# Optimization experiments

Measured on AMD Instinct MI355X. Metric: run time of the kernel, lower is better.

## Reference

```python
import jax, jax.numpy as jnp
import numpy as np

DT = 0.01      # timestep
RE = 0.001     # 'Re' coefficient in source
NLEVEL = 5     # multigrid levels
D, H, W = 96, 192, 192  # nz, ny, nx interior grid


def _conv(x, w, stride=1):
    # 1->1 channel 3D stencil conv, VALID padding (matches Conv3d padding=0, bias=0)
    return jax.lax.conv_general_dilated(
        x, w, (stride,) * 3, 'VALID',
        dimension_numbers=('NCDHW', 'OIDHW', 'NCDHW'))


def _pad(x):
    # BC application + halo exchange collapsed to zero halo (single-device reference)
    return jnp.pad(x, ((0, 0), (0, 0), (1, 1), (1, 1), (1, 1)))


def _prol(x):
    # nn.Upsample(scale_factor=2, mode='nearest')
    for ax in (2, 3, 4):
        x = jnp.repeat(x, 2, axis=ax)
    return x


def _stencils():
    wA = np.zeros((1, 1, 3, 3, 3), np.float32)
    wA[0, 0, 1, 1, 1] = -6.0
    for d in range(3):
        idx = [1, 1, 1]
        idx[d] = 0; wA[(0, 0, *idx)] = 1.0
        idx[d] = 2; wA[(0, 0, *idx)] = 1.0
    w_diff = wA.copy()
    w_x = np.zeros((1, 1, 3, 3, 3), np.float32); w_x[0, 0, 1, 1, 0] = -0.5; w_x[0, 0, 1, 1, 2] = 0.5
    w_y = np.zeros((1, 1, 3, 3, 3), np.float32); w_y[0, 0, 1, 0, 1] = -0.5; w_y[0, 0, 1, 2, 1] = 0.5
    w_z = np.zeros((1, 1, 3, 3, 3), np.float32); w_z[0, 0, 0, 1, 1] = -0.5; w_z[0, 0, 2, 1, 1] = 0.5
    w_res = np.full((1, 1, 2, 2, 2), 0.125, np.float32)
    return tuple(jnp.asarray(a) for a in (wA, w_diff, w_x, w_y, w_z, w_res))


def setup_inputs() -> dict:
    key = jax.random.key(0)
    ks = jax.random.split(key, 5)
    shape = (1, 1, D, H, W)
    wA, w_diff, w_xadv, w_yadv, w_zadv, w_res = _stencils()
    return {
        'values_u': jax.random.normal(ks[0], shape, jnp.float32),
        'values_v': jax.random.normal(ks[1], shape, jnp.float32),
        'values_w': jax.random.normal(ks[2], shape, jnp.float32),
        'values_p': jax.random.normal(ks[3], shape, jnp.float32),
        'sigma': jax.random.uniform(ks[4], shape, jnp.float32),
        'wA': wA, 'w_diff': w_diff, 'w_xadv': w_xadv,
        'w_yadv': w_yadv, 'w_zadv': w_zadv, 'w_res': w_res,
        'iteration': 2,
    }


def _forward(values_u, values_v, values_w, values_p, sigma,
             wA, w_diff, w_xadv, w_yadv, w_zadv, w_res, iteration):
    diag = wA[0, 0, 1, 1, 1]
    A = lambda x: _conv(x, wA)
    diff = lambda x: _conv(x, w_diff)
    xadv = lambda x: _conv(x, w_xadv)
    yadv = lambda x: _conv(x, w_yadv)
    zadv = lambda x: _conv(x, w_zadv)
    res = lambda x: _conv(x, w_res, stride=2)

    inv = 1.0 / (1.0 + DT * sigma)           # solid_body (LIBM) damping
    sb = lambda a, b, c: (a * inv, b * inv, c * inv)

    def pg(uu, vv, ww, u, v, w_):
        # PG_vector with k_u = k_v = k_w = ones
        kpp = _pad(jnp.ones_like(u))
        ku = 0.5 * (diff(uu) + diff(uu * kpp) - u * diff(kpp))
        kv = 0.5 * (diff(vv) + diff(vv * kpp) - v * diff(kpp))
        kw = 0.5 * (diff(ww) + diff(ww * kpp) - w_ * diff(kpp))
        return ku, kv, kw

    u, v, w_ = sb(values_u, values_v, values_w)
    uu, vv, ww, pp = _pad(u), _pad(v), _pad(w_), _pad(values_p)

    ku, kv, kw = pg(uu, vv, ww, u, v, w_)
    b_u = u + 0.5 * (RE * ku * DT - u * xadv(uu) * DT - v * yadv(uu) * DT - w_ * zadv(uu) * DT) - xadv(pp) * DT
    b_v = v + 0.5 * (RE * kv * DT - u * xadv(vv) * DT - v * yadv(vv) * DT - w_ * zadv(vv) * DT) - yadv(pp) * DT
    b_w = w_ + 0.5 * (RE * kw * DT - u * xadv(ww) * DT - v * yadv(ww) * DT - w_ * zadv(ww) * DT) - zadv(pp) * DT
    b_u, b_v, b_w = sb(b_u, b_v, b_w)
    buu, bvv, bww = _pad(b_u), _pad(b_v), _pad(b_w)

    ku, kv, kw = pg(buu, bvv, bww, b_u, b_v, b_w)
    u = u + RE * ku * DT - b_u * xadv(buu) * DT - b_v * yadv(buu) * DT - b_w * zadv(buu) * DT - xadv(pp) * DT
    v = v + RE * kv * DT - b_u * xadv(bvv) * DT - b_v * yadv(bvv) * DT - b_w * zadv(bvv) * DT - yadv(pp) * DT
    w_ = w_ + RE * kw * DT - b_u * xadv(bww) * DT - b_v * yadv(bww) * DT - b_w * zadv(bww) * DT - zadv(pp) * DT
    u, v, w_ = sb(u, v, w_)
    uu, vv, ww = _pad(u), _pad(v), _pad(w_)

    # F_cycle_MG: multigrid pressure solve
    b = -(xadv(uu) + yadv(vv) + zadv(ww)) / DT
    p = values_p
    for _ in range(iteration):
        wmg = jnp.zeros((1, 1, 1, 1, 1), p.dtype)
        r = A(pp) - b
        r_s = [r]
        for _i in range(1, NLEVEL - 1):
            r = res(r)
            r_s.append(r)
        for i in reversed(range(1, NLEVEL - 1)):
            wmg = wmg - A(_pad(wmg)) / diag + r_s[i] / diag  # Jacobi smooth (broadcasts at coarsest)
            wmg = _prol(wmg)
        p = p - wmg
        p = p - A(pp) / diag + b / diag
        pp = _pad(p)

    u = u - xadv(pp) * DT
    v = v - yadv(pp) * DT
    w_ = w_ - zadv(pp) * DT
    u, v, w_ = sb(u, v, w_)
    return u, v, w_, p, wmg, r


def reference(values_u, values_v, values_w, values_p, sigma,
              wA, w_diff, w_xadv, w_yadv, w_zadv, w_res, iteration):
    return _forward(values_u, values_v, values_w, values_p, sigma,
                    wA, w_diff, w_xadv, w_yadv, w_zadv, w_res, iteration)
```

## Files before the change

kernel.cpp:

```cpp
#include <hip/hip_runtime.h>

#define DZc 96
#define HYc 192
#define WXc 192
#define SHs (WXc)
#define SDs (HYc*WXc)
#define NTOT (DZc*HYc*WXc)
#define DTc 0.01f
#define REc 0.001f

#define D1 48
#define H1 96
#define W1 96
#define N1 (D1*H1*W1)
#define D2 24
#define H2 48
#define W2 48
#define N2 (D2*H2*W2)
#define D3 12
#define H3 24
#define W3 24
#define N3 (D3*H3*W3)


struct Row6 { float a[6]; };

struct Geo {
  int base, il, ir, iym, iyp, izm, izp;
  float mxl, mxr, mym, myp, mzm, mzp;
};

__device__ __forceinline__ Geo mkgeo(int x0,int y,int z){
  Geo g;
  g.base = (z*HYc + y)*WXc + x0;
  bool hxm=x0>0, hxp=x0<WXc-4, hym=y>0, hyp=y<HYc-1, hzm=z>0, hzp=z<DZc-1;
  g.il  = hxm ? g.base-1   : g.base;  g.ir  = hxp ? g.base+4   : g.base;
  g.iym = hym ? g.base-SHs : g.base;  g.iyp = hyp ? g.base+SHs : g.base;
  g.izm = hzm ? g.base-SDs : g.base;  g.izp = hzp ? g.base+SDs : g.base;
  g.mxl = hxm?1.f:0.f; g.mxr = hxp?1.f:0.f;
  g.mym = hym?1.f:0.f; g.myp = hyp?1.f:0.f;
  g.mzm = hzm?1.f:0.f; g.mzp = hzp?1.f:0.f;
  return g;
}

__device__ __forceinline__ Row6 ld6(const float* __restrict__ f, const Geo& g){
  Row6 r;
  float4 c = *reinterpret_cast<const float4*>(f + g.base);
  r.a[0]=f[g.il]*g.mxl; r.a[1]=c.x; r.a[2]=c.y; r.a[3]=c.z; r.a[4]=c.w; r.a[5]=f[g.ir]*g.mxr;
  return r;
}
__device__ __forceinline__ void ld4a(const float* __restrict__ f, int idx, float* o){
  float4 c = *reinterpret_cast<const float4*>(f + idx);
  o[0]=c.x; o[1]=c.y; o[2]=c.z; o[3]=c.w;
}

struct Sten { Row6 c; float ym[4], yp[4], zm[4], zp[4]; };
__device__ __forceinline__ Sten ldsten(const float* __restrict__ f, const Geo& g){
  Sten s;
  s.c = ld6(f,g);
  ld4a(f,g.iym,s.ym); ld4a(f,g.iyp,s.yp); ld4a(f,g.izm,s.zm); ld4a(f,g.izp,s.zp);
  return s;
}

__device__ __forceinline__ void restrict_body(
    const float rv[4], int x0,
    float (*l0)[4][192], float (*l1)[2][96],
    float* __restrict__ r1p, float* __restrict__ r2p,
    int by, int bz){
  *reinterpret_cast<float4*>(&l0[threadIdx.z][threadIdx.y][x0]) =
      make_float4(rv[0],rv[1],rv[2],rv[3]);
  __syncthreads();
  int t = (threadIdx.z*4 + threadIdx.y)*48 + threadIdx.x;
  if (t < 384){
    int xc = t % 96, yc = (t/96)&1, zc = t/192;
    float s = 0.f;
    for (int a=0;a<2;a++)
      for (int bq=0;bq<2;bq++)
        s += l0[2*zc+a][2*yc+bq][2*xc] + l0[2*zc+a][2*yc+bq][2*xc+1];
    float r1v = 0.125f*s;
    r1p[((bz*2+zc)*H1 + (by*2+yc))*W1 + xc] = r1v;
    l1[zc][yc][xc] = r1v;
  }
  __syncthreads();
  if (t < 48){
    float s = 0.f;
    for (int a=0;a<2;a++)
      for (int bq=0;bq<2;bq++)
        s += l1[a][bq][2*t] + l1[a][bq][2*t+1];
    r2p[(bz*H2 + by)*W2 + t] = 0.125f*s;
  }
}

__global__ __launch_bounds__(192) void k_pred(
    const float* __restrict__ vu, const float* __restrict__ vv,
    const float* __restrict__ vw, const float* __restrict__ sig,
    const float* __restrict__ p,
    float* __restrict__ bu, float* __restrict__ bv, float* __restrict__ bw){
  int x0 = threadIdx.x*4, y = blockIdx.y*4 + threadIdx.y, z = blockIdx.z;
  Geo g = mkgeo(x0,y,z);

  Sten S = ldsten(sig,g);
  Sten U = ldsten(vu,g);
  Sten V = ldsten(vv,g);
  Sten W = ldsten(vw,g);
  Sten P = ldsten(p,g);

  float iv6[6], du6[6], dv6[6], dw6[6];
  #pragma unroll
  for (int i=0;i<6;i++){
    iv6[i] = 1.f/(1.f + DTc*S.c.a[i]);
    du6[i] = U.c.a[i]*iv6[i]; dv6[i] = V.c.a[i]*iv6[i]; dw6[i] = W.c.a[i]*iv6[i];
  }
  float duym[4],duyp[4],duzm[4],duzp[4];
  float dvym[4],dvyp[4],dvzm[4],dvzp[4];
  float dwym[4],dwyp[4],dwzm[4],dwzp[4];
  #pragma unroll
  for (int e=0;e<4;e++){
    float iym = g.mym/(1.f + DTc*S.ym[e]);
    float iyp = g.myp/(1.f + DTc*S.yp[e]);
    float izm = g.mzm/(1.f + DTc*S.zm[e]);
    float izp = g.mzp/(1.f + DTc*S.zp[e]);
    duym[e]=U.ym[e]*iym; duyp[e]=U.yp[e]*iyp; duzm[e]=U.zm[e]*izm; duzp[e]=U.zp[e]*izp;
    dvym[e]=V.ym[e]*iym; dvyp[e]=V.yp[e]*iyp; dvzm[e]=V.zm[e]*izm; dvzp[e]=V.zp[e]*izp;
    dwym[e]=W.ym[e]*iym; dwyp[e]=W.yp[e]*iyp; dwzm[e]=W.zm[e]*izm; dwzp[e]=W.zp[e]*izp;
  }

  float rbu[4], rbv[4], rbw[4];
  #pragma unroll
  for (int e=0;e<4;e++){
    const float exm = (e==0)?g.mxl:1.f, exp_ = (e==3)?g.mxr:1.f;
    const float me = (1.f-exm)+(1.f-exp_)+(1.f-g.mym)+(1.f-g.myp)+(1.f-g.mzm)+(1.f-g.mzp);
    float uc=du6[e+1], vc=dv6[e+1], wc=dw6[e+1];
    float ku = (du6[e]+du6[e+2]+duym[e]+duyp[e]+duzm[e]+duzp[e] - 6.f*uc) + 0.5f*me*uc;
    float kv = (dv6[e]+dv6[e+2]+dvym[e]+dvyp[e]+dvzm[e]+dvzp[e] - 6.f*vc) + 0.5f*me*vc;
    float kw = (dw6[e]+dw6[e+2]+dwym[e]+dwyp[e]+dwzm[e]+dwzp[e] - 6.f*wc) + 0.5f*me*wc;
    float advu = uc*0.5f*(du6[e+2]-du6[e]) + vc*0.5f*(duyp[e]-duym[e]) + wc*0.5f*(duzp[e]-duzm[e]);
    float advv = uc*0.5f*(dv6[e+2]-dv6[e]) + vc*0.5f*(dvyp[e]-dvym[e]) + wc*0.5f*(dvzp[e]-dvzm[e]);
    float advw = uc*0.5f*(dw6[e+2]-dw6[e]) + vc*0.5f*(dwyp[e]-dwym[e]) + wc*0.5f*(dwzp[e]-dwzm[e]);
    float gpx = 0.5f*(P.c.a[e+2]-P.c.a[e]);
    float gpy = 0.5f*(P.yp[e]*g.myp - P.ym[e]*g.mym);
    float gpz = 0.5f*(P.zp[e]*g.mzp - P.zm[e]*g.mzm);
    rbu[e] = (uc + 0.5f*(REc*ku*DTc - advu*DTc) - gpx*DTc)*iv6[e+1];
    rbv[e] = (vc + 0.5f*(REc*kv*DTc - advv*DTc) - gpy*DTc)*iv6[e+1];
    rbw[e] = (wc + 0.5f*(REc*kw*DTc - advw*DTc) - gpz*DTc)*iv6[e+1];
  }
  *reinterpret_cast<float4*>(bu+g.base) = make_float4(rbu[0],rbu[1],rbu[2],rbu[3]);
  *reinterpret_cast<float4*>(bv+g.base) = make_float4(rbv[0],rbv[1],rbv[2],rbv[3]);
  *reinterpret_cast<float4*>(bw+g.base) = make_float4(rbw[0],rbw[1],rbw[2],rbw[3]);
}

__global__ __launch_bounds__(192) void k_corr(
    const float* __restrict__ bu, const float* __restrict__ bv,
    const float* __restrict__ bw, const float* __restrict__ p,
    const float* __restrict__ vu, const float* __restrict__ vv,
    const float* __restrict__ vw, const float* __restrict__ sig,
    float* __restrict__ u, float* __restrict__ v, float* __restrict__ w){
  int x0 = threadIdx.x*4, y = blockIdx.y*4 + threadIdx.y, z = blockIdx.z;
  Geo g = mkgeo(x0,y,z);

  Sten BU = ldsten(bu,g);
  Sten BV = ldsten(bv,g);
  Sten BW = ldsten(bw,g);
  Sten P  = ldsten(p,g);
  float cu[4],cv[4],cw[4],cs[4];
  ld4a(vu,g.base,cu); ld4a(vv,g.base,cv); ld4a(vw,g.base,cw); ld4a(sig,g.base,cs);

  float ru[4], rv[4], rw[4];
  #pragma unroll
  for (int e=0;e<4;e++){
    const float exm = (e==0)?g.mxl:1.f, exp_ = (e==3)?g.mxr:1.f;
    const float me = (1.f-exm)+(1.f-exp_)+(1.f-g.mym)+(1.f-g.myp)+(1.f-g.mzm)+(1.f-g.mzp);
    float ivc = 1.f/(1.f + DTc*cs[e]);
    float buc=BU.c.a[e+1], bvc=BV.c.a[e+1], bwc=BW.c.a[e+1];
    float buym=BU.ym[e]*g.mym, buyp=BU.yp[e]*g.myp, buzm=BU.zm[e]*g.mzm, buzp=BU.zp[e]*g.mzp;
    float bvym=BV.ym[e]*g.mym, bvyp=BV.yp[e]*g.myp, bvzm=BV.zm[e]*g.mzm, bvzp=BV.zp[e]*g.mzp;
    float bwym=BW.ym[e]*g.mym, bwyp=BW.yp[e]*g.myp, bwzm=BW.zm[e]*g.mzm, bwzp=BW.zp[e]*g.mzp;
    float ku = (BU.c.a[e]+BU.c.a[e+2]+buym+buyp+buzm+buzp - 6.f*buc) + 0.5f*me*buc;
    float kv = (BV.c.a[e]+BV.c.a[e+2]+bvym+bvyp+bvzm+bvzp - 6.f*bvc) + 0.5f*me*bvc;
    float kw = (BW.c.a[e]+BW.c.a[e+2]+bwym+bwyp+bwzm+bwzp - 6.f*bwc) + 0.5f*me*bwc;
    float advu = buc*0.5f*(BU.c.a[e+2]-BU.c.a[e]) + bvc*0.5f*(buyp-buym) + bwc*0.5f*(buzp-buzm);
    float advv = buc*0.5f*(BV.c.a[e+2]-BV.c.a[e]) + bvc*0.5f*(bvyp-bvym) + bwc*0.5f*(bvzp-bvzm);
    float advw = buc*0.5f*(BW.c.a[e+2]-BW.c.a[e]) + bvc*0.5f*(bwyp-bwym) + bwc*0.5f*(bwzp-bwzm);
    float gpx = 0.5f*(P.c.a[e+2]-P.c.a[e]);
    float gpy = 0.5f*(P.yp[e]*g.myp - P.ym[e]*g.mym);
    float gpz = 0.5f*(P.zp[e]*g.mzp - P.zm[e]*g.mzm);
    ru[e] = (cu[e]*ivc + REc*ku*DTc - advu*DTc - gpx*DTc)*ivc;
    rv[e] = (cv[e]*ivc + REc*kv*DTc - advv*DTc - gpy*DTc)*ivc;
    rw[e] = (cw[e]*ivc + REc*kw*DTc - advw*DTc - gpz*DTc)*ivc;
  }
  *reinterpret_cast<float4*>(u+g.base) = make_float4(ru[0],ru[1],ru[2],ru[3]);
  *reinterpret_cast<float4*>(v+g.base) = make_float4(rv[0],rv[1],rv[2],rv[3]);
  *reinterpret_cast<float4*>(w+g.base) = make_float4(rw[0],rw[1],rw[2],rw[3]);
}

__global__ __launch_bounds__(768) void k_res1(
    const float* __restrict__ u, const float* __restrict__ v,
    const float* __restrict__ w, const float* __restrict__ p,
    float* __restrict__ r0, float* __restrict__ r1, float* __restrict__ r2){
  __shared__ float l0[4][4][192];
  __shared__ float l1[2][2][96];
  int x0 = threadIdx.x*4;
  int y = blockIdx.y*4 + threadIdx.y;
  int z = blockIdx.z*4 + threadIdx.z;
  Geo g = mkgeo(x0,y,z);

  Row6 u6 = ld6(u,g);
  float vym[4],vyp[4],wzm[4],wzp[4];
  ld4a(v,g.iym,vym); ld4a(v,g.iyp,vyp); ld4a(w,g.izm,wzm); ld4a(w,g.izp,wzp);
  Sten P = ldsten(p,g);

  float rv[4];
  #pragma unroll
  for (int e=0;e<4;e++){
    float b = -(0.5f*(u6.a[e+2]-u6.a[e])
              + 0.5f*(vyp[e]*g.myp - vym[e]*g.mym)
              + 0.5f*(wzp[e]*g.mzp - wzm[e]*g.mzm)) * (1.f/DTc);
    float lap = P.c.a[e]+P.c.a[e+2]
              + P.ym[e]*g.mym + P.yp[e]*g.myp + P.zm[e]*g.mzm + P.zp[e]*g.mzp
              - 6.f*P.c.a[e+1];
    rv[e] = lap - b;
  }
  *reinterpret_cast<float4*>(r0+g.base) = make_float4(rv[0],rv[1],rv[2],rv[3]);
  restrict_body(rv, x0, l0, l1, r1, r2, blockIdx.y, blockIdx.z);
}

__global__ __launch_bounds__(768) void k_res2(
    const float* __restrict__ vp, const float* __restrict__ r0,
    const float* __restrict__ w1,
    float* __restrict__ p1, float* __restrict__ r0b,
    float* __restrict__ r1b, float* __restrict__ r2b){
  __shared__ float l0[4][4][192];
  __shared__ float l1[2][2][96];
  int x0 = threadIdx.x*4;
  int y = blockIdx.y*4 + threadIdx.y;
  int z = blockIdx.z*4 + threadIdx.z;
  Geo g = mkgeo(x0,y,z);

  Sten R = ldsten(r0,g);
  float vpa[4]; ld4a(vp,g.base,vpa);

  int cz=z>>1, cy=y>>1, cx0=x0>>1;
  const float* wrow = w1 + (cz*H1+cy)*W1;
  int icxm = (x0>0)? cx0-1 : cx0;
  int icxp = (x0<WXc-4)? cx0+2 : cx0+1;
  float wc0=wrow[icxm], wc1=wrow[cx0], wc2=wrow[cx0+1], wc3=wrow[icxp];
  int cym_=(y>0)?((y-1)>>1):cy, cyp_=(y<HYc-1)?((y+1)>>1):cy;
  int czm_=(z>0)?((z-1)>>1):cz, czp_=(z<DZc-1)?((z+1)>>1):cz;
  const float* rym_r = w1 + (cz*H1+cym_)*W1;
  const float* ryp_r = w1 + (cz*H1+cyp_)*W1;
  const float* rzm_r = w1 + (czm_*H1+cy)*W1;
  const float* rzp_r = w1 + (czp_*H1+cy)*W1;
  float wym0=rym_r[cx0], wym1=rym_r[cx0+1];
  float wyp0=ryp_r[cx0], wyp1=ryp_r[cx0+1];
  float wzm0=rzm_r[cx0], wzm1=rzm_r[cx0+1];
  float wzp0=rzp_r[cx0], wzp1=rzp_r[cx0+1];

  float rv[4], pv[4];
  #pragma unroll
  for (int e=0;e<4;e++){
    const float exm = (e==0)?g.mxl:1.f, exp_ = (e==3)?g.mxr:1.f;
    float tc  = (e<2)? wc1 : wc2;
    float txm = ((e==0)? wc0 : (e<3)? wc1 : wc2)*exm;
    float txp = ((e==0)? wc1 : (e<3)? wc2 : wc3)*exp_;
    float tym = ((e<2)? wym0 : wym1)*g.mym, typ = ((e<2)? wyp0 : wyp1)*g.myp;
    float tzm = ((e<2)? wzm0 : wzm1)*g.mzm, tzp = ((e<2)? wzp0 : wzp1)*g.mzp;
    float lapw = txm+txp+tym+typ+tzm+tzp - 6.f*tc;
    float lapr = R.c.a[e]+R.c.a[e+2]
               + R.ym[e]*g.mym + R.yp[e]*g.myp + R.zm[e]*g.mzm + R.zp[e]*g.mzp
               - 6.f*R.c.a[e+1];
    rv[e] = R.c.a[e+1] + lapr*(1.f/6.f) - lapw;
    pv[e] = vpa[e] - tc + R.c.a[e+1]*(1.f/6.f);
  }
  *reinterpret_cast<float4*>(p1 +g.base) = make_float4(pv[0],pv[1],pv[2],pv[3]);
  *reinterpret_cast<float4*>(r0b+g.base) = make_float4(rv[0],rv[1],rv[2],rv[3]);
  restrict_body(rv, x0, l0, l1, r1b, r2b, blockIdx.y, blockIdx.z);
}

__global__ void k_lvl2(const float* __restrict__ r2, float* __restrict__ w2o,
                       float* __restrict__ r3o){
  int idx = blockIdx.x*256 + threadIdx.x;
  if (idx >= N2) return;
  int x = idx % W2; int tt = idx / W2; int y = tt % H2; int z = tt / H2;
  int cx = x>>1, cy = y>>1, cz = z>>1;
  auto r3eval = [&](int az,int ay,int ax)->float{
    int fi = ((2*az)*H2 + 2*ay)*W2 + 2*ax;
    return 0.125f*(r2[fi] + r2[fi+1] + r2[fi+W2] + r2[fi+W2+1]
                 + r2[fi+H2*W2] + r2[fi+H2*W2+1] + r2[fi+H2*W2+W2] + r2[fi+H2*W2+W2+1]);
  };
  float mxm=(x>0)?1.f:0.f, mxp=(x<W2-1)?1.f:0.f;
  float mym=(y>0)?1.f:0.f, myp=(y<H2-1)?1.f:0.f;
  float mzm=(z>0)?1.f:0.f, mzp=(z<D2-1)?1.f:0.f;
  int cxm=(x>0)?(x-1)>>1:0, cxp=(x<W2-1)?(x+1)>>1:cx;
  int cym=(y>0)?(y-1)>>1:0, cyp=(y<H2-1)?(y+1)>>1:cy;
  int czm=(z>0)?(z-1)>>1:0, czp=(z<D2-1)?(z+1)>>1:cz;
  const float k6 = -1.f/6.f;
  float r3c = r3eval(cz,cy,cx);
  float tc  = r3c*k6;
  float txm = r3eval(cz,cy,cxm)*k6*mxm, txp = r3eval(cz,cy,cxp)*k6*mxp;
  float tym = r3eval(cz,cym,cx)*k6*mym, typ = r3eval(cz,cyp,cx)*k6*myp;
  float tzm = r3eval(czm,cy,cx)*k6*mzm, tzp = r3eval(czp,cy,cx)*k6*mzp;
  float lapt = txm+txp+tym+typ+tzm+tzp - 6.f*tc;
  w2o[idx] = tc + lapt*(1.f/6.f) - r2[idx]*(1.f/6.f);
  if (((x|y|z)&1)==0) r3o[(cz*H3+cy)*W3+cx] = r3c;
}

__global__ void k_lvl1(const float* __restrict__ w2, const float* __restrict__ r1,
                       float* __restrict__ w1o){
  int idx = blockIdx.x*256 + threadIdx.x;
  if (idx >= N1) return;
  int x = idx % W1; int tt = idx / W1; int y = tt % H1; int z = tt / H1;
  int cx = x>>1, cy = y>>1, cz = z>>1;
  float mxm=(x>0)?1.f:0.f, mxp=(x<W1-1)?1.f:0.f;
  float mym=(y>0)?1.f:0.f, myp=(y<H1-1)?1.f:0.f;
  float mzm=(z>0)?1.f:0.f, mzp=(z<D1-1)?1.f:0.f;
  int cxm=(x>0)?(x-1)>>1:0, cxp=(x<W1-1)?(x+1)>>1:cx;
  int cym=(y>0)?(y-1)>>1:0, cyp=(y<H1-1)?(y+1)>>1:cy;
  int czm=(z>0)?(z-1)>>1:0, czp=(z<D1-1)?(z+1)>>1:cz;
  auto A = [&](int az,int ay,int ax)->float{ return w2[(az*H2+ay)*W2+ax]; };
  float tc = A(cz,cy,cx);
  float txm = A(cz,cy,cxm)*mxm, txp = A(cz,cy,cxp)*mxp;
  float tym = A(cz,cym,cx)*mym, typ = A(cz,cyp,cx)*myp;
  float tzm = A(czm,cy,cx)*mzm, tzp = A(czp,cy,cx)*mzp;
  float lapt = txm+txp+tym+typ+tzm+tzp - 6.f*tc;
  w1o[idx] = tc + lapt*(1.f/6.f) - r1[idx]*(1.f/6.f);
}

__global__ __launch_bounds__(192) void k_final(
    const float* __restrict__ p1, const float* __restrict__ r0b,
    const float* __restrict__ w1b,
    const float* __restrict__ u, const float* __restrict__ v,
    const float* __restrict__ w, const float* __restrict__ sig,
    float* __restrict__ ou, float* __restrict__ ov, float* __restrict__ ow,
    float* __restrict__ op, float* __restrict__ owmg){
  int x0 = threadIdx.x*4, y = blockIdx.y*4 + threadIdx.y, z = blockIdx.z;
  Geo g = mkgeo(x0,y,z);

  Sten P = ldsten(p1,g);
  Sten R = ldsten(r0b,g);
  float cu[4],cv[4],cw[4],cs[4];
  ld4a(u,g.base,cu); ld4a(v,g.base,cv); ld4a(w,g.base,cw); ld4a(sig,g.base,cs);

  int cz=z>>1, cy=y>>1, cx0=x0>>1;
  const float* wrow = w1b + (cz*H1+cy)*W1;
  int icxm = (x0>0)? cx0-1 : cx0;
  int icxp = (x0<WXc-4)? cx0+2 : cx0+1;
  float wc0=wrow[icxm], wc1=wrow[cx0], wc2=wrow[cx0+1], wc3=wrow[icxp];
  int cym_=(y>0)?((y-1)>>1):cy, cyp_=(y<HYc-1)?((y+1)>>1):cy;
  int czm_=(z>0)?((z-1)>>1):cz, czp_=(z<DZc-1)?((z+1)>>1):cz;
  const float* rym_r = w1b + (cz*H1+cym_)*W1;
  const float* ryp_r = w1b + (cz*H1+cyp_)*W1;
  const float* rzm_r = w1b + (czm_*H1+cy)*W1;
  const float* rzp_r = w1b + (czp_*H1+cy)*W1;
  float wym0=rym_r[cx0], wym1=rym_r[cx0+1];
  float wyp0=ryp_r[cx0], wyp1=ryp_r[cx0+1];
  float wzm0=rzm_r[cx0], wzm1=rzm_r[cx0+1];
  float wzp0=rzp_r[cx0], wzp1=rzp_r[cx0+1];

  float rou[4], rov[4], row_[4], rop[4], rowm[4];
  #pragma unroll
  for (int e=0;e<4;e++){
    const float exm = (e==0)?g.mxl:1.f, exp_ = (e==3)?g.mxr:1.f;
    float tc  = (e<2)? wc1 : wc2;
    float txm = (e==0)? wc0 : (e<3)? wc1 : wc2;
    float txp = (e==0)? wc1 : (e<3)? wc2 : wc3;
    float tym = (e<2)? wym0 : wym1, typ = (e<2)? wyp0 : wyp1;
    float tzm = (e<2)? wzm0 : wzm1, tzp = (e<2)? wzp0 : wzp1;
    float p2xm = (P.c.a[e]   + R.c.a[e]  *(1.f/6.f) - txm)*exm;
    float p2xp = (P.c.a[e+2] + R.c.a[e+2]*(1.f/6.f) - txp)*exp_;
    float p2ym = (P.ym[e] + R.ym[e]*(1.f/6.f) - tym)*g.mym;
    float p2yp = (P.yp[e] + R.yp[e]*(1.f/6.f) - typ)*g.myp;
    float p2zm = (P.zm[e] + R.zm[e]*(1.f/6.f) - tzm)*g.mzm;
    float p2zp = (P.zp[e] + R.zp[e]*(1.f/6.f) - tzp)*g.mzp;
    float pc = P.c.a[e+1] - tc + R.c.a[e+1]*(1.f/6.f);
    float iv = 1.f/(1.f + DTc*cs[e]);
    rop[e]  = pc;
    rowm[e] = tc;
    rou[e] = (cu[e] - 0.5f*(p2xp-p2xm)*DTc)*iv;
    rov[e] = (cv[e] - 0.5f*(p2yp-p2ym)*DTc)*iv;
    row_[e]= (cw[e] - 0.5f*(p2zp-p2zm)*DTc)*iv;
  }
  *reinterpret_cast<float4*>(ou+g.base)   = make_float4(rou[0],rou[1],rou[2],rou[3]);
  *reinterpret_cast<float4*>(ov+g.base)   = make_float4(rov[0],rov[1],rov[2],rov[3]);
  *reinterpret_cast<float4*>(ow+g.base)   = make_float4(row_[0],row_[1],row_[2],row_[3]);
  *reinterpret_cast<float4*>(op+g.base)   = make_float4(rop[0],rop[1],rop[2],rop[3]);
  *reinterpret_cast<float4*>(owmg+g.base) = make_float4(rowm[0],rowm[1],rowm[2],rowm[3]);
}

extern "C" void kernel_launch(void* const* d_in, const int* in_sizes, int n_in,
                              void* d_out, int out_size, void* d_ws, size_t ws_size,
                              hipStream_t stream){
  const float* vu  = (const float*)d_in[0];
  const float* vv  = (const float*)d_in[1];
  const float* vw  = (const float*)d_in[2];
  const float* vp  = (const float*)d_in[3];
  const float* sig = (const float*)d_in[4];

  const size_t N = (size_t)NTOT;
  float* ws   = (float*)d_ws;
  float* u    = ws;
  float* v    = ws + N;
  float* w    = ws + 2*N;
  float* bu   = ws + 3*N;
  float* bv   = ws + 4*N;
  float* bw   = ws + 5*N;
  float* r0b  = ws + 6*N;
  float* r1   = ws + 7*N;
  float* r2   = r1 + N1;
  float* w2   = r2 + N2;
  float* w1   = w2 + N2;

  float* out     = (float*)d_out;
  float* out_u   = out;
  float* out_v   = out + N;
  float* out_w   = out + 2*N;
  float* out_p   = out + 3*N;
  float* out_wmg = out + 4*N;
  float* out_r   = out + 5*N;

  dim3 bA(48,4,1), gA(1, HYc/4, DZc);
  dim3 bR(48,4,4), gR(1, HYc/4, DZc/4);

  k_pred<<<gA,bA,0,stream>>>(vu,vv,vw,sig,vp,bu,bv,bw);
  k_corr<<<gA,bA,0,stream>>>(bu,bv,bw,vp,vu,vv,vw,sig,u,v,w);

  float* r0 = bv; float* p1 = bw;
  k_res1<<<gR,bR,0,stream>>>(u,v,w,vp,r0,r1,r2);
  k_lvl2<<<(N2+255)/256,256,0,stream>>>(r2,w2,out_r);
  k_lvl1<<<(N1+255)/256,256,0,stream>>>(w2,r1,w1);

  k_res2<<<gR,bR,0,stream>>>(vp,r0,w1,p1,r0b,r1,r2);
  k_lvl2<<<(N2+255)/256,256,0,stream>>>(r2,w2,out_r);
  k_lvl1<<<(N1+255)/256,256,0,stream>>>(w2,r1,w1);

  k_final<<<gA,bA,0,stream>>>(p1,r0b,w1,u,v,w,sig,out_u,out_v,out_w,out_p,out_wmg);
}
```

Before: 247.0 us.

## Interleave predictor outputs as AoS and fold p1/r0b into single q field

The predictor now writes bu/bv/bw interleaved into one array, so the corrector reads each stencil neighbour as three contiguous float4 loads instead of three separate streams. k_res2 also algebraically combines the updated pressure and the residual/6 term into a single field q, so it writes one array instead of two. k_final then reads one stencil instead of two. This cuts global memory traffic, at the cost of uncoalesced-ish scalar x-halo loads in the AoS layout and a slightly different float rounding order.

```diff
diff --git a/kernel.cpp b/kernel.cpp
--- a/kernel.cpp
+++ b/kernel.cpp
@@ -29,7 +29,6 @@
   int base, il, ir, iym, iyp, izm, izp;
   float mxl, mxr, mym, myp, mzm, mzp;
 };
-
 __device__ __forceinline__ Geo mkgeo(int x0,int y,int z){
   Geo g;
   g.base = (z*HYc + y)*WXc + x0;
@@ -42,7 +41,6 @@
   g.mzm = hzm?1.f:0.f; g.mzp = hzp?1.f:0.f;
   return g;
 }
-
 __device__ __forceinline__ Row6 ld6(const float* __restrict__ f, const Geo& g){
   Row6 r;
   float4 c = *reinterpret_cast<const float4*>(f + g.base);
@@ -53,13 +51,116 @@
   float4 c = *reinterpret_cast<const float4*>(f + idx);
   o[0]=c.x; o[1]=c.y; o[2]=c.z; o[3]=c.w;
 }
-
+__device__ __forceinline__ void ld12(const float* __restrict__ f, int idx, float* o){
+  ld4a(f,idx,o); ld4a(f,idx+4,o+4); ld4a(f,idx+8,o+8);
+}
 struct Sten { Row6 c; float ym[4], yp[4], zm[4], zp[4]; };
 __device__ __forceinline__ Sten ldsten(const float* __restrict__ f, const Geo& g){
   Sten s;
   s.c = ld6(f,g);
   ld4a(f,g.iym,s.ym); ld4a(f,g.iyp,s.yp); ld4a(f,g.izm,s.zm); ld4a(f,g.izp,s.zp);
   return s;
+}
+
+__global__ __launch_bounds__(192) void k_pred(
+    const float* __restrict__ vu, const float* __restrict__ vv,
+    const float* __restrict__ vw, const float* __restrict__ sig,
+    const float* __restrict__ p, float* __restrict__ B){
+  int x0 = threadIdx.x*4, y = blockIdx.y*4 + threadIdx.y, z = blockIdx.z;
+  Geo g = mkgeo(x0,y,z);
+
+  Sten S = ldsten(sig,g);
+  Sten U = ldsten(vu,g);
+  Sten V = ldsten(vv,g);
+  Sten W = ldsten(vw,g);
+  Sten P = ldsten(p,g);
+
+  float iv6[6], du6[6], dv6[6], dw6[6];
+  #pragma unroll
+  for (int i=0;i<6;i++){
+    iv6[i] = 1.f/(1.f + DTc*S.c.a[i]);
+    du6[i] = U.c.a[i]*iv6[i]; dv6[i] = V.c.a[i]*iv6[i]; dw6[i] = W.c.a[i]*iv6[i];
+  }
+  float ob[12];
+  #pragma unroll
+  for (int e=0;e<4;e++){
+    float iym = g.mym/(1.f + DTc*S.ym[e]);
+    float iyp = g.myp/(1.f + DTc*S.yp[e]);
+    float izm = g.mzm/(1.f + DTc*S.zm[e]);
+    float izp = g.mzp/(1.f + DTc*S.zp[e]);
+    float uym=U.ym[e]*iym, uyp=U.yp[e]*iyp, uzm=U.zm[e]*izm, uzp=U.zp[e]*izp;
+    float vym=V.ym[e]*iym, vyp=V.yp[e]*iyp, vzm=V.zm[e]*izm, vzp=V.zp[e]*izp;
+    float wym=W.ym[e]*iym, wyp=W.yp[e]*iyp, wzm=W.zm[e]*izm, wzp=W.zp[e]*izp;
+    const float exm = (e==0)?g.mxl:1.f, exp_ = (e==3)?g.mxr:1.f;
+    const float me = (1.f-exm)+(1.f-exp_)+(1.f-g.mym)+(1.f-g.myp)+(1.f-g.mzm)+(1.f-g.mzp);
+    float uc=du6[e+1], vc=dv6[e+1], wc=dw6[e+1];
+    float ku = (du6[e]+du6[e+2]+uym+uyp+uzm+uzp - 6.f*uc) + 0.5f*me*uc;
+    float kv = (dv6[e]+dv6[e+2]+vym+vyp+vzm+vzp - 6.f*vc) + 0.5f*me*vc;
+    float kw = (dw6[e]+dw6[e+2]+wym+wyp+wzm+wzp - 6.f*wc) + 0.5f*me*wc;
+    float advu = uc*0.5f*(du6[e+2]-du6[e]) + vc*0.5f*(uyp-uym) + wc*0.5f*(uzp-uzm);
+    float advv = uc*0.5f*(dv6[e+2]-dv6[e]) + vc*0.5f*(vyp-vym) + wc*0.5f*(vzp-vzm);
+    float advw = uc*0.5f*(dw6[e+2]-dw6[e]) + vc*0.5f*(wyp-wym) + wc*0.5f*(wzp-wzm);
+    float gpx = 0.5f*(P.c.a[e+2]-P.c.a[e]);
+    float gpy = 0.5f*(P.yp[e]*g.myp - P.ym[e]*g.mym);
+    float gpz = 0.5f*(P.zp[e]*g.mzp - P.zm[e]*g.mzm);
+    ob[3*e+0] = (uc + 0.5f*(REc*ku*DTc - advu*DTc) - gpx*DTc)*iv6[e+1];
+    ob[3*e+1] = (vc + 0.5f*(REc*kv*DTc - advv*DTc) - gpy*DTc)*iv6[e+1];
+    ob[3*e+2] = (wc + 0.5f*(REc*kw*DTc - advw*DTc) - gpz*DTc)*iv6[e+1];
+  }
+  int ib = 3*g.base;
+  *reinterpret_cast<float4*>(B+ib)   = make_float4(ob[0],ob[1],ob[2],ob[3]);
+  *reinterpret_cast<float4*>(B+ib+4) = make_float4(ob[4],ob[5],ob[6],ob[7]);
+  *reinterpret_cast<float4*>(B+ib+8) = make_float4(ob[8],ob[9],ob[10],ob[11]);
+}
+
+__global__ __launch_bounds__(192) void k_corr(
+    const float* __restrict__ B, const float* __restrict__ p,
+    const float* __restrict__ vu, const float* __restrict__ vv,
+    const float* __restrict__ vw, const float* __restrict__ sig,
+    float* __restrict__ u, float* __restrict__ v, float* __restrict__ w){
+  int x0 = threadIdx.x*4, y = blockIdx.y*4 + threadIdx.y, z = blockIdx.z;
+  Geo g = mkgeo(x0,y,z);
+
+  float f0[12], fym[12], fyp[12], fzm[12], fzp[12];
+  ld12(B, 3*g.base, f0);
+  ld12(B, 3*g.iym, fym); ld12(B, 3*g.iyp, fyp);
+  ld12(B, 3*g.izm, fzm); ld12(B, 3*g.izp, fzp);
+  float eL0 = B[3*g.il]*g.mxl,   eL1 = B[3*g.il+1]*g.mxl,   eL2 = B[3*g.il+2]*g.mxl;
+  float eR0 = B[3*g.ir]*g.mxr,   eR1 = B[3*g.ir+1]*g.mxr,   eR2 = B[3*g.ir+2]*g.mxr;
+  float BUr[6]={eL0,f0[0],f0[3],f0[6],f0[9],eR0};
+  float BVr[6]={eL1,f0[1],f0[4],f0[7],f0[10],eR1};
+  float BWr[6]={eL2,f0[2],f0[5],f0[8],f0[11],eR2};
+
+  Sten P  = ldsten(p,g);
+  float cu[4],cv[4],cw[4],cs[4];
+  ld4a(vu,g.base,cu); ld4a(vv,g.base,cv); ld4a(vw,g.base,cw); ld4a(sig,g.base,cs);
+
+  float ru[4], rv[4], rw[4];
+  #pragma unroll
+  for (int e=0;e<4;e++){
+    const float exm = (e==0)?g.mxl:1.f, exp_ = (e==3)?g.mxr:1.f;
+    const float me = (1.f-exm)+(1.f-exp_)+(1.f-g.mym)+(1.f-g.myp)+(1.f-g.mzm)+(1.f-g.mzp);
+    float ivc = 1.f/(1.f + DTc*cs[e]);
+    float buc=BUr[e+1], bvc=BVr[e+1], bwc=BWr[e+1];
+    float buym=fym[3*e]*g.mym,   buyp=fyp[3*e]*g.myp,   buzm=fzm[3*e]*g.mzm,   buzp=fzp[3*e]*g.mzp;
+    float bvym=fym[3*e+1]*g.mym, bvyp=fyp[3*e+1]*g.myp, bvzm=fzm[3*e+1]*g.mzm, bvzp=fzp[3*e+1]*g.mzp;
+    float bwym=fym[3*e+2]*g.mym, bwyp=fyp[3*e+2]*g.myp, bwzm=fzm[3*e+2]*g.mzm, bwzp=fzp[3*e+2]*g.mzp;
+    float ku = (BUr[e]+BUr[e+2]+buym+buyp+buzm+buzp - 6.f*buc) + 0.5f*me*buc;
+    float kv = (BVr[e]+BVr[e+2]+bvym+bvyp+bvzm+bvzp - 6.f*bvc) + 0.5f*me*bvc;
+    float kw = (BWr[e]+BWr[e+2]+bwym+bwyp+bwzm+bwzp - 6.f*bwc) + 0.5f*me*bwc;
+    float advu = buc*0.5f*(BUr[e+2]-BUr[e]) + bvc*0.5f*(buyp-buym) + bwc*0.5f*(buzp-buzm);
+    float advv = buc*0.5f*(BVr[e+2]-BVr[e]) + bvc*0.5f*(bvyp-bvym) + bwc*0.5f*(bvzp-bvzm);
+    float advw = buc*0.5f*(BWr[e+2]-BWr[e]) + bvc*0.5f*(bwyp-bwym) + bwc*0.5f*(bwzp-bwzm);
+    float gpx = 0.5f*(P.c.a[e+2]-P.c.a[e]);
+    float gpy = 0.5f*(P.yp[e]*g.myp - P.ym[e]*g.mym);
+    float gpz = 0.5f*(P.zp[e]*g.mzp - P.zm[e]*g.mzm);
+    ru[e] = (cu[e]*ivc + REc*ku*DTc - advu*DTc - gpx*DTc)*ivc;
+    rv[e] = (cv[e]*ivc + REc*kv*DTc - advv*DTc - gpy*DTc)*ivc;
+    rw[e] = (cw[e]*ivc + REc*kw*DTc - advw*DTc - gpz*DTc)*ivc;
+  }
+  *reinterpret_cast<float4*>(u+g.base) = make_float4(ru[0],ru[1],ru[2],ru[3]);
+  *reinterpret_cast<float4*>(v+g.base) = make_float4(rv[0],rv[1],rv[2],rv[3]);
+  *reinterpret_cast<float4*>(w+g.base) = make_float4(rw[0],rw[1],rw[2],rw[3]);
 }
 
 __device__ __forceinline__ void restrict_body(
@@ -91,108 +192,6 @@
   }
 }
 
-__global__ __launch_bounds__(192) void k_pred(
-    const float* __restrict__ vu, const float* __restrict__ vv,
-    const float* __restrict__ vw, const float* __restrict__ sig,
-    const float* __restrict__ p,
-    float* __restrict__ bu, float* __restrict__ bv, float* __restrict__ bw){
-  int x0 = threadIdx.x*4, y = blockIdx.y*4 + threadIdx.y, z = blockIdx.z;
-  Geo g = mkgeo(x0,y,z);
-
-  Sten S = ldsten(sig,g);
-  Sten U = ldsten(vu,g);
-  Sten V = ldsten(vv,g);
-  Sten W = ldsten(vw,g);
-  Sten P = ldsten(p,g);
-
-  float iv6[6], du6[6], dv6[6], dw6[6];
-  #pragma unroll
-  for (int i=0;i<6;i++){
-    iv6[i] = 1.f/(1.f + DTc*S.c.a[i]);
-    du6[i] = U.c.a[i]*iv6[i]; dv6[i] = V.c.a[i]*iv6[i]; dw6[i] = W.c.a[i]*iv6[i];
-  }
-  float duym[4],duyp[4],duzm[4],duzp[4];
-  float dvym[4],dvyp[4],dvzm[4],dvzp[4];
-  float dwym[4],dwyp[4],dwzm[4],dwzp[4];
-  #pragma unroll
-  for (int e=0;e<4;e++){
-    float iym = g.mym/(1.f + DTc*S.ym[e]);
-    float iyp = g.myp/(1.f + DTc*S.yp[e]);
-    float izm = g.mzm/(1.f + DTc*S.zm[e]);
-    float izp = g.mzp/(1.f + DTc*S.zp[e]);
-    duym[e]=U.ym[e]*iym; duyp[e]=U.yp[e]*iyp; duzm[e]=U.zm[e]*izm; duzp[e]=U.zp[e]*izp;
-    dvym[e]=V.ym[e]*iym; dvyp[e]=V.yp[e]*iyp; dvzm[e]=V.zm[e]*izm; dvzp[e]=V.zp[e]*izp;
-    dwym[e]=W.ym[e]*iym; dwyp[e]=W.yp[e]*iyp; dwzm[e]=W.zm[e]*izm; dwzp[e]=W.zp[e]*izp;
-  }
-
-  float rbu[4], rbv[4], rbw[4];
-  #pragma unroll
-  for (int e=0;e<4;e++){
-    const float exm = (e==0)?g.mxl:1.f, exp_ = (e==3)?g.mxr:1.f;
-    const float me = (1.f-exm)+(1.f-exp_)+(1.f-g.mym)+(1.f-g.myp)+(1.f-g.mzm)+(1.f-g.mzp);
-    float uc=du6[e+1], vc=dv6[e+1], wc=dw6[e+1];
-    float ku = (du6[e]+du6[e+2]+duym[e]+duyp[e]+duzm[e]+duzp[e] - 6.f*uc) + 0.5f*me*uc;
-    float kv = (dv6[e]+dv6[e+2]+dvym[e]+dvyp[e]+dvzm[e]+dvzp[e] - 6.f*vc) + 0.5f*me*vc;
-    float kw = (dw6[e]+dw6[e+2]+dwym[e]+dwyp[e]+dwzm[e]+dwzp[e] - 6.f*wc) + 0.5f*me*wc;
-    float advu = uc*0.5f*(du6[e+2]-du6[e]) + vc*0.5f*(duyp[e]-duym[e]) + wc*0.5f*(duzp[e]-duzm[e]);
-    float advv = uc*0.5f*(dv6[e+2]-dv6[e]) + vc*0.5f*(dvyp[e]-dvym[e]) + wc*0.5f*(dvzp[e]-dvzm[e]);
-    float advw = uc*0.5f*(dw6[e+2]-dw6[e]) + vc*0.5f*(dwyp[e]-dwym[e]) + wc*0.5f*(dwzp[e]-dwzm[e]);
-    float gpx = 0.5f*(P.c.a[e+2]-P.c.a[e]);
-    float gpy = 0.5f*(P.yp[e]*g.myp - P.ym[e]*g.mym);
-    float gpz = 0.5f*(P.zp[e]*g.mzp - P.zm[e]*g.mzm);
-    rbu[e] = (uc + 0.5f*(REc*ku*DTc - advu*DTc) - gpx*DTc)*iv6[e+1];
-    rbv[e] = (vc + 0.5f*(REc*kv*DTc - advv*DTc) - gpy*DTc)*iv6[e+1];
-    rbw[e] = (wc + 0.5f*(REc*kw*DTc - advw*DTc) - gpz*DTc)*iv6[e+1];
-  }
-  *reinterpret_cast<float4*>(bu+g.base) = make_float4(rbu[0],rbu[1],rbu[2],rbu[3]);
-  *reinterpret_cast<float4*>(bv+g.base) = make_float4(rbv[0],rbv[1],rbv[2],rbv[3]);
-  *reinterpret_cast<float4*>(bw+g.base) = make_float4(rbw[0],rbw[1],rbw[2],rbw[3]);
-}
-
-__global__ __launch_bounds__(192) void k_corr(
-    const float* __restrict__ bu, const float* __restrict__ bv,
-    const float* __restrict__ bw, const float* __restrict__ p,
-    const float* __restrict__ vu, const float* __restrict__ vv,
-    const float* __restrict__ vw, const float* __restrict__ sig,
-    float* __restrict__ u, float* __restrict__ v, float* __restrict__ w){
-  int x0 = threadIdx.x*4, y = blockIdx.y*4 + threadIdx.y, z = blockIdx.z;
-  Geo g = mkgeo(x0,y,z);
-
-  Sten BU = ldsten(bu,g);
-  Sten BV = ldsten(bv,g);
-  Sten BW = ldsten(bw,g);
-  Sten P  = ldsten(p,g);
-  float cu[4],cv[4],cw[4],cs[4];
-  ld4a(vu,g.base,cu); ld4a(vv,g.base,cv); ld4a(vw,g.base,cw); ld4a(sig,g.base,cs);
-
-  float ru[4], rv[4], rw[4];
-  #pragma unroll
-  for (int e=0;e<4;e++){
-    const float exm = (e==0)?g.mxl:1.f, exp_ = (e==3)?g.mxr:1.f;
-    const float me = (1.f-exm)+(1.f-exp_)+(1.f-g.mym)+(1.f-g.myp)+(1.f-g.mzm)+(1.f-g.mzp);
-    float ivc = 1.f/(1.f + DTc*cs[e]);
-    float buc=BU.c.a[e+1], bvc=BV.c.a[e+1], bwc=BW.c.a[e+1];
-    float buym=BU.ym[e]*g.mym, buyp=BU.yp[e]*g.myp, buzm=BU.zm[e]*g.mzm, buzp=BU.zp[e]*g.mzp;
-    float bvym=BV.ym[e]*g.mym, bvyp=BV.yp[e]*g.myp, bvzm=BV.zm[e]*g.mzm, bvzp=BV.zp[e]*g.mzp;
-    float bwym=BW.ym[e]*g.mym, bwyp=BW.yp[e]*g.myp, bwzm=BW.zm[e]*g.mzm, bwzp=BW.zp[e]*g.mzp;
-    float ku = (BU.c.a[e]+BU.c.a[e+2]+buym+buyp+buzm+buzp - 6.f*buc) + 0.5f*me*buc;
-    float kv = (BV.c.a[e]+BV.c.a[e+2]+bvym+bvyp+bvzm+bvzp - 6.f*bvc) + 0.5f*me*bvc;
-    float kw = (BW.c.a[e]+BW.c.a[e+2]+bwym+bwyp+bwzm+bwzp - 6.f*bwc) + 0.5f*me*bwc;
-    float advu = buc*0.5f*(BU.c.a[e+2]-BU.c.a[e]) + bvc*0.5f*(buyp-buym) + bwc*0.5f*(buzp-buzm);
-    float advv = buc*0.5f*(BV.c.a[e+2]-BV.c.a[e]) + bvc*0.5f*(bvyp-bvym) + bwc*0.5f*(bvzp-bvzm);
-    float advw = buc*0.5f*(BW.c.a[e+2]-BW.c.a[e]) + bvc*0.5f*(bwyp-bwym) + bwc*0.5f*(bwzp-bwzm);
-    float gpx = 0.5f*(P.c.a[e+2]-P.c.a[e]);
-    float gpy = 0.5f*(P.yp[e]*g.myp - P.ym[e]*g.mym);
-    float gpz = 0.5f*(P.zp[e]*g.mzp - P.zm[e]*g.mzm);
-    ru[e] = (cu[e]*ivc + REc*ku*DTc - advu*DTc - gpx*DTc)*ivc;
-    rv[e] = (cv[e]*ivc + REc*kv*DTc - advv*DTc - gpy*DTc)*ivc;
-    rw[e] = (cw[e]*ivc + REc*kw*DTc - advw*DTc - gpz*DTc)*ivc;
-  }
-  *reinterpret_cast<float4*>(u+g.base) = make_float4(ru[0],ru[1],ru[2],ru[3]);
-  *reinterpret_cast<float4*>(v+g.base) = make_float4(rv[0],rv[1],rv[2],rv[3]);
-  *reinterpret_cast<float4*>(w+g.base) = make_float4(rw[0],rw[1],rw[2],rw[3]);
-}
-
 __global__ __launch_bounds__(768) void k_res1(
     const float* __restrict__ u, const float* __restrict__ v,
     const float* __restrict__ w, const float* __restrict__ p,
@@ -227,8 +226,7 @@
 __global__ __launch_bounds__(768) void k_res2(
     const float* __restrict__ vp, const float* __restrict__ r0,
     const float* __restrict__ w1,
-    float* __restrict__ p1, float* __restrict__ r0b,
-    float* __restrict__ r1b, float* __restrict__ r2b){
+    float* __restrict__ q, float* __restrict__ r1b, float* __restrict__ r2b){
   __shared__ float l0[4][4][192];
   __shared__ float l1[2][2][96];
   int x0 = threadIdx.x*4;
@@ -255,7 +253,7 @@
   float wzm0=rzm_r[cx0], wzm1=rzm_r[cx0+1];
   float wzp0=rzp_r[cx0], wzp1=rzp_r[cx0+1];
 
-  float rv[4], pv[4];
+  float rv[4], qv[4];
   #pragma unroll
   for (int e=0;e<4;e++){
     const float exm = (e==0)?g.mxl:1.f, exp_ = (e==3)?g.mxr:1.f;
@@ -265,14 +263,12 @@
     float tym = ((e<2)? wym0 : wym1)*g.mym, typ = ((e<2)? wyp0 : wyp1)*g.myp;
     float tzm = ((e<2)? wzm0 : wzm1)*g.mzm, tzp = ((e<2)? wzp0 : wzp1)*g.mzp;
     float lapw = txm+txp+tym+typ+tzm+tzp - 6.f*tc;
-    float lapr = R.c.a[e]+R.c.a[e+2]
-               + R.ym[e]*g.mym + R.yp[e]*g.myp + R.zm[e]*g.mzm + R.zp[e]*g.mzp
-               - 6.f*R.c.a[e+1];
-    rv[e] = R.c.a[e+1] + lapr*(1.f/6.f) - lapw;
-    pv[e] = vpa[e] - tc + R.c.a[e+1]*(1.f/6.f);
-  }
-  *reinterpret_cast<float4*>(p1 +g.base) = make_float4(pv[0],pv[1],pv[2],pv[3]);
-  *reinterpret_cast<float4*>(r0b+g.base) = make_float4(rv[0],rv[1],rv[2],rv[3]);
+    float sumnb = R.c.a[e]+R.c.a[e+2]
+                + R.ym[e]*g.mym + R.yp[e]*g.myp + R.zm[e]*g.mzm + R.zp[e]*g.mzp;
+    rv[e] = sumnb*(1.f/6.f) - lapw;
+    qv[e] = vpa[e] - tc + R.c.a[e+1]*(1.f/6.f) + rv[e]*(1.f/6.f);
+  }
+  *reinterpret_cast<float4*>(q+g.base) = make_float4(qv[0],qv[1],qv[2],qv[3]);
   restrict_body(rv, x0, l0, l1, r1b, r2b, blockIdx.y, blockIdx.z);
 }
 
@@ -326,8 +322,7 @@
 }
 
 __global__ __launch_bounds__(192) void k_final(
-    const float* __restrict__ p1, const float* __restrict__ r0b,
-    const float* __restrict__ w1b,
+    const float* __restrict__ q, const float* __restrict__ w1b,
     const float* __restrict__ u, const float* __restrict__ v,
     const float* __restrict__ w, const float* __restrict__ sig,
     float* __restrict__ ou, float* __restrict__ ov, float* __restrict__ ow,
@@ -335,8 +330,7 @@
   int x0 = threadIdx.x*4, y = blockIdx.y*4 + threadIdx.y, z = blockIdx.z;
   Geo g = mkgeo(x0,y,z);
 
-  Sten P = ldsten(p1,g);
-  Sten R = ldsten(r0b,g);
+  Sten Q = ldsten(q,g);
   float cu[4],cv[4],cw[4],cs[4];
   ld4a(u,g.base,cu); ld4a(v,g.base,cv); ld4a(w,g.base,cw); ld4a(sig,g.base,cs);
 
@@ -365,13 +359,13 @@
     float txp = (e==0)? wc1 : (e<3)? wc2 : wc3;
     float tym = (e<2)? wym0 : wym1, typ = (e<2)? wyp0 : wyp1;
     float tzm = (e<2)? wzm0 : wzm1, tzp = (e<2)? wzp0 : wzp1;
-    float p2xm = (P.c.a[e]   + R.c.a[e]  *(1.f/6.f) - txm)*exm;
-    float p2xp = (P.c.a[e+2] + R.c.a[e+2]*(1.f/6.f) - txp)*exp_;
-    float p2ym = (P.ym[e] + R.ym[e]*(1.f/6.f) - tym)*g.mym;
-    float p2yp = (P.yp[e] + R.yp[e]*(1.f/6.f) - typ)*g.myp;
-    float p2zm = (P.zm[e] + R.zm[e]*(1.f/6.f) - tzm)*g.mzm;
-    float p2zp = (P.zp[e] + R.zp[e]*(1.f/6.f) - tzp)*g.mzp;
-    float pc = P.c.a[e+1] - tc + R.c.a[e+1]*(1.f/6.f);
+    float p2xm = (Q.c.a[e]   - txm)*exm;
+    float p2xp = (Q.c.a[e+2] - txp)*exp_;
+    float p2ym = (Q.ym[e] - tym)*g.mym;
+    float p2yp = (Q.yp[e] - typ)*g.myp;
+    float p2zm = (Q.zm[e] - tzm)*g.mzm;
+    float p2zp = (Q.zp[e] - tzp)*g.mzp;
+    float pc = Q.c.a[e+1] - tc;
     float iv = 1.f/(1.f + DTc*cs[e]);
     rop[e]  = pc;
     rowm[e] = tc;
@@ -400,14 +394,13 @@
   float* u    = ws;
   float* v    = ws + N;
   float* w    = ws + 2*N;
-  float* bu   = ws + 3*N;
-  float* bv   = ws + 4*N;
-  float* bw   = ws + 5*N;
-  float* r0b  = ws + 6*N;
+  float* B    = ws + 3*N;
+  float* r0   = ws + 6*N;
   float* r1   = ws + 7*N;
   float* r2   = r1 + N1;
   float* w2   = r2 + N2;
   float* w1   = w2 + N2;
+  float* q    = B;
 
   float* out     = (float*)d_out;
   float* out_u   = out;
@@ -420,17 +413,16 @@
   dim3 bA(48,4,1), gA(1, HYc/4, DZc);
   dim3 bR(48,4,4), gR(1, HYc/4, DZc/4);
 
-  k_pred<<<gA,bA,0,stream>>>(vu,vv,vw,sig,vp,bu,bv,bw);
-  k_corr<<<gA,bA,0,stream>>>(bu,bv,bw,vp,vu,vv,vw,sig,u,v,w);
-
-  float* r0 = bv; float* p1 = bw;
+  k_pred<<<gA,bA,0,stream>>>(vu,vv,vw,sig,vp,B);
+  k_corr<<<gA,bA,0,stream>>>(B,vp,vu,vv,vw,sig,u,v,w);
+
   k_res1<<<gR,bR,0,stream>>>(u,v,w,vp,r0,r1,r2);
   k_lvl2<<<(N2+255)/256,256,0,stream>>>(r2,w2,out_r);
   k_lvl1<<<(N1+255)/256,256,0,stream>>>(w2,r1,w1);
 
-  k_res2<<<gR,bR,0,stream>>>(vp,r0,w1,p1,r0b,r1,r2);
+  k_res2<<<gR,bR,0,stream>>>(vp,r0,w1,q,r1,r2);
   k_lvl2<<<(N2+255)/256,256,0,stream>>>(r2,w2,out_r);
   k_lvl1<<<(N1+255)/256,256,0,stream>>>(w2,r1,w1);
 
-  k_final<<<gA,bA,0,stream>>>(p1,r0b,w1,u,v,w,sig,out_u,out_v,out_w,out_p,out_wmg);
-}
+  k_final<<<gA,bA,0,stream>>>(q,w1,u,v,w,sig,out_u,out_v,out_w,out_p,out_wmg);
+}
```

Measured after the change: 251.1 us. No clear change (+1.7%).
